# Performance work log

Measured on AMD Instinct MI355X. Metric: run time of the kernel, lower is better.

Reference implementation:

```python
import jax, jax.numpy as jnp
import numpy as np

N_WORDS = 500000
N_LABELS = 64
PAD_INDEX = 0
UNK_INDEX = 1
BATCH, SEQ_LEN = 8192, 512


def setup_inputs() -> dict:
    key = jax.random.key(0)
    kw, kl, klen = jax.random.split(key, 3)
    # sequence lengths in [S/2, S]; pads go at the end (loop semantics assume contiguous prefix)
    lens = jax.random.randint(klen, (BATCH,), SEQ_LEN // 2, SEQ_LEN + 1)
    words = jax.random.randint(kw, (BATCH, SEQ_LEN), 2, N_WORDS, dtype=jnp.int32)
    labels = jax.random.randint(kl, (BATCH, SEQ_LEN), 0, N_LABELS, dtype=jnp.int32)
    pos = jnp.arange(SEQ_LEN, dtype=jnp.int32)[None, :]
    words = jnp.where(pos < lens[:, None], words, PAD_INDEX)
    trans_count = jnp.zeros((N_LABELS + 1, N_LABELS + 1), jnp.float32)
    emit_count = jnp.zeros((N_WORDS, N_LABELS), jnp.float32)
    return {"words": words, "labels": labels,
            "trans_count": trans_count, "emit_count": emit_count}


def reference(words, labels, trans_count, emit_count):
    # Vectorized equivalent of the double Python loop of scalar increments.
    B, S = words.shape
    lens = (words != PAD_INDEX).sum(-1)                       # [B]
    valid = jnp.arange(S, dtype=lens.dtype)[None, :] < lens[:, None]  # [B,S]
    wgt = valid.astype(trans_count.dtype).ravel()             # 1.0 for counted tokens
    ext_words = jnp.where(words >= N_WORDS, UNK_INDEX, words)
    # pre label: -1 (== last index N_LABELS) at j=0, else labels[:, j-1]
    pre = jnp.concatenate(
        [jnp.full((B, 1), N_LABELS, labels.dtype), labels[:, :-1]], axis=1)
    # trans_count[t, pre] += 1  (flattened scatter-add)
    t_flat = (labels.astype(jnp.int32) * (N_LABELS + 1) + pre.astype(jnp.int32)).ravel()
    tc = trans_count.ravel().at[t_flat].add(wgt).reshape(trans_count.shape)
    # emit_count[w, t] += 1
    e_flat = (ext_words.astype(jnp.int32) * N_LABELS + labels.astype(jnp.int32)).ravel()
    ec = emit_count.ravel().at[e_flat].add(wgt).reshape(emit_count.shape)
    return tc, ec
```

## Files before the change

### kernel.cpp

```cpp
#include <hip/hip_runtime.h>
#include <hip/hip_bf16.h>


constexpr int N_WORDS  = 500000;
constexpr int N_LABELS = 64;
constexpr int SEQ_LEN  = 512;
constexpr int BINS     = (N_LABELS + 1) * (N_LABELS + 1);
constexpr int N_CELLS  = N_WORDS * N_LABELS;
constexpr int P        = 1025;
constexpr int CPP      = 31232;
constexpr int CAP      = 8192;
constexpr int B1 = 1024, G1 = 512;
constexpr int TILE_TOK = 8192;
constexpr int B2 = 1024;
constexpr int FIN_BLOCKS = 5;


__global__ __launch_bounds__(B1)
void phase1(const int* __restrict__ words, const int* __restrict__ labels,
            unsigned* __restrict__ cursors,
            unsigned short* __restrict__ keys,
            unsigned* __restrict__ part_t,
            int n) {
    __shared__ unsigned trans[BINS];
    __shared__ unsigned keybuf[TILE_TOK];
    __shared__ unsigned cnt[P];
    __shared__ unsigned base[P];
    __shared__ unsigned pos[P];
    for (int k = threadIdx.x; k < BINS; k += B1) trans[k] = 0u;
    __syncthreads();

    const int nquads = n >> 2;
    const int qpt    = TILE_TOK >> 2;
    const int ntiles = (nquads + qpt - 1) / qpt;

    for (int tile = blockIdx.x; tile < ntiles; tile += gridDim.x) {
        const int q0     = tile * qpt;
        const int tquads = min(qpt, nquads - q0);

        for (int k = threadIdx.x; k < P; k += B1) { cnt[k] = 0u; pos[k] = 0u; }
        __syncthreads();

        for (int lq = threadIdx.x; lq < tquads; lq += B1) {
            const int q = q0 + lq;
            const int i = q << 2;
            const int4 w4 = reinterpret_cast<const int4*>(words)[q];
            const int4 l4 = reinterpret_cast<const int4*>(labels)[q];
            const int j0 = i & (SEQ_LEN - 1);
            int pre = (j0 == 0) ? N_LABELS : labels[i - 1];
            int wv[4] = {w4.x, w4.y, w4.z, w4.w};
            int lv[4] = {l4.x, l4.y, l4.z, l4.w};
            #pragma unroll
            for (int k = 0; k < 4; ++k) {
                const int lab = lv[k];
                unsigned pack = 0xFFFFFFFFu;
                if (wv[k] != 0) {
                    atomicAdd(&trans[lab * (N_LABELS + 1) + pre], 1u);
                    const int w = (wv[k] >= N_WORDS) ? 1 : wv[k];
                    const unsigned key = (unsigned)w * N_LABELS + (unsigned)lab;
                    const unsigned p   = key / CPP;
                    pack = (p << 16) | (key - p * CPP);
                    atomicAdd(&cnt[p], 1u);
                }
                keybuf[(lq << 2) + k] = pack;
                pre = lab;
            }
        }
        __syncthreads();

        for (int p = threadIdx.x; p < P; p += B1) {
            const unsigned c = cnt[p];
            base[p] = c ? atomicAdd(&cursors[p], c) : 0u;
        }
        __syncthreads();

        const int ttok = tquads << 2;
        for (int t = threadIdx.x; t < ttok; t += B1) {
            const unsigned pack = keybuf[t];
            if (pack != 0xFFFFFFFFu) {
                const unsigned p   = pack >> 16;
                const unsigned loc = pack & 0xFFFFu;
                const unsigned slot = base[p] + atomicAdd(&pos[p], 1u);
                if (slot < CAP)
                    keys[(size_t)p * CAP + slot] = (unsigned short)loc;
            }
        }
        __syncthreads();
    }

    unsigned* my = part_t + (size_t)blockIdx.x * BINS;
    for (int k = threadIdx.x; k < BINS; k += B1) my[k] = trans[k];
}


__global__ __launch_bounds__(B2)
void phase2(const unsigned* __restrict__ cursors,
            const unsigned short* __restrict__ keys,
            const unsigned* __restrict__ part_t,
            float* __restrict__ out) {
    extern __shared__ unsigned h[];
    const unsigned bid = blockIdx.x;

    if (bid >= (unsigned)P) {
        const int k = (bid - P) * B2 + threadIdx.x;
        if (k < BINS) {
            unsigned s = 0;
            #pragma unroll 8
            for (int pb = 0; pb < G1; ++pb) s += part_t[(size_t)pb * BINS + k];
            out[k] = (float)s;
        }
        return;
    }

    float* __restrict__ emit = out + BINS;
    const unsigned base_cell = bid * (unsigned)CPP;
    const unsigned cells = min((unsigned)CPP, (unsigned)N_CELLS - base_cell);
    const unsigned n32 = (cells + 1u) >> 1;
    unsigned nk = cursors[bid]; if (nk > CAP) nk = CAP;
    const unsigned short* kp = keys + (size_t)bid * CAP;

    for (unsigned j = threadIdx.x; j < n32; j += B2) h[j] = 0u;
    __syncthreads();
    for (unsigned i = threadIdx.x; i < nk; i += B2) {
        const unsigned c = kp[i];
        atomicAdd(&h[c >> 1], (c & 1u) ? 65536u : 1u);
    }
    __syncthreads();
    for (unsigned j = threadIdx.x; j < cells; j += B2) {
        const unsigned v = h[j >> 1];
        const unsigned c = (j & 1u) ? (v >> 16) : (v & 0xFFFFu);
        emit[base_cell + j] = (float)c;
    }
}


__global__ __launch_bounds__(256)
void zero_kernel(uint4* __restrict__ out, int out_quads, int out_size) {
    const uint4 z = {0u, 0u, 0u, 0u};
    const int stride = gridDim.x * blockDim.x;
    for (int q = blockIdx.x * blockDim.x + threadIdx.x; q < out_quads; q += stride)
        out[q] = z;
    if (blockIdx.x == 0 && threadIdx.x < (out_size & 3))
        ((unsigned*)out)[(out_quads << 2) + threadIdx.x] = 0u;
}

__global__ __launch_bounds__(1024)
void count_fallback(const int* __restrict__ words, const int* __restrict__ labels,
                    float* __restrict__ out, int nquads) {
    __shared__ unsigned hist[BINS];
    for (int k = threadIdx.x; k < BINS; k += 1024) hist[k] = 0u;
    __syncthreads();
    float* __restrict__ emit = out + BINS;
    const int stride = gridDim.x * blockDim.x;
    for (int q = blockIdx.x * blockDim.x + threadIdx.x; q < nquads; q += stride) {
        const int i = q << 2;
        const int4 w4 = reinterpret_cast<const int4*>(words)[q];
        const int4 l4 = reinterpret_cast<const int4*>(labels)[q];
        const int j0 = i & (SEQ_LEN - 1);
        int pre = (j0 == 0) ? N_LABELS : labels[i - 1];
        int wv[4] = {w4.x, w4.y, w4.z, w4.w};
        int lv[4] = {l4.x, l4.y, l4.z, l4.w};
        #pragma unroll
        for (int k = 0; k < 4; ++k) {
            const int w = wv[k], lab = lv[k];
            if (w != 0) {
                atomicAdd(&hist[lab * (N_LABELS + 1) + pre], 1u);
                const int we = (w >= N_WORDS) ? 1 : w;
                atomicAdd(&emit[(size_t)we * N_LABELS + lab], 1.0f);
            }
            pre = lab;
        }
    }
    __syncthreads();
    for (int k = threadIdx.x; k < 1024 * 8 && k < BINS; k += 1024) {}
    for (int k = threadIdx.x; k < BINS; k += 1024) {
        const unsigned c = hist[k];
        if (c) atomicAdd(&out[k], (float)c);
    }
}


extern "C" void kernel_launch(void* const* d_in, const int* in_sizes, int n_in,
                              void* d_out, int out_size, void* d_ws, size_t ws_size,
                              hipStream_t stream) {
    const int* words  = (const int*)d_in[0];
    const int* labels = (const int*)d_in[1];
    float* out = (float*)d_out;

    const int n = in_sizes[0];

    const size_t cur_off   = 0;
    const size_t key_off   = 8192;
    const size_t key_bytes = (size_t)P * CAP * sizeof(unsigned short);
    const size_t part_off  = key_off + key_bytes;
    const size_t part_bytes = (size_t)G1 * BINS * sizeof(unsigned);
    const size_t need = part_off + part_bytes;

    if (ws_size >= need) {
        unsigned* cursors    = (unsigned*)((char*)d_ws + cur_off);
        unsigned short* keys = (unsigned short*)((char*)d_ws + key_off);
        unsigned* part_t     = (unsigned*)((char*)d_ws + part_off);

        hipMemsetAsync(cursors, 0, P * sizeof(unsigned), stream);
        phase1<<<G1, B1, 0, stream>>>(words, labels, cursors, keys, part_t, n);
        phase2<<<P + FIN_BLOCKS, B2, (CPP / 2) * sizeof(unsigned), stream>>>(
            cursors, keys, part_t, out);
    } else {
        const int out_quads = out_size >> 2;
        zero_kernel<<<2048, 256, 0, stream>>>((uint4*)d_out, out_quads, out_size);
        count_fallback<<<512, 1024, 0, stream>>>(words, labels, out, n >> 2);
    }
}
```

Before: 273.9 us.

## Fuse bucketing and histogram phases into one cooperative kernel with grid sync

Replaces the memset plus two kernel launches with a single cooperative kernel. It zeroes the cursors, buckets the keys, does a grid-wide sync, and then builds per-partition LDS histograms with float4 output stores. The partition count changes to 1000 with 32000 cells each, and the grid is sized from occupancy. This removes launch overhead and the tail between phases, at the cost of fewer resident blocks during the histogram phase and the expense of grid syncs. The large dynamic LDS is now also allocated during phase 1.

```diff
diff --git a/kernel.cpp b/kernel.cpp
--- a/kernel.cpp
+++ b/kernel.cpp
@@ -1,47 +1,54 @@
 #include <hip/hip_runtime.h>
-#include <hip/hip_bf16.h>
+#include <hip/hip_cooperative_groups.h>
+
+namespace cg = cooperative_groups;
 
 
 constexpr int N_WORDS  = 500000;
 constexpr int N_LABELS = 64;
 constexpr int SEQ_LEN  = 512;
 constexpr int BINS     = (N_LABELS + 1) * (N_LABELS + 1);
-constexpr int N_CELLS  = N_WORDS * N_LABELS;
-constexpr int P        = 1025;
-constexpr int CPP      = 31232;
+constexpr int P        = 1000;
+constexpr int CPP      = 32000;
 constexpr int CAP      = 8192;
-constexpr int B1 = 1024, G1 = 512;
+constexpr int B        = 1024;
+constexpr int MAXG     = 512;
 constexpr int TILE_TOK = 8192;
-constexpr int B2 = 1024;
-constexpr int FIN_BLOCKS = 5;
-
-
-__global__ __launch_bounds__(B1)
-void phase1(const int* __restrict__ words, const int* __restrict__ labels,
-            unsigned* __restrict__ cursors,
-            unsigned short* __restrict__ keys,
-            unsigned* __restrict__ part_t,
-            int n) {
-    __shared__ unsigned trans[BINS];
-    __shared__ unsigned keybuf[TILE_TOK];
-    __shared__ unsigned cnt[P];
-    __shared__ unsigned base[P];
-    __shared__ unsigned pos[P];
-    for (int k = threadIdx.x; k < BINS; k += B1) trans[k] = 0u;
-    __syncthreads();
+constexpr int QPT      = TILE_TOK / 4;
+constexpr size_t DYN_BYTES = (size_t)(CPP / 2) * 4;
+
+
+__global__ __launch_bounds__(B)
+void fused(const int* __restrict__ words, const int* __restrict__ labels,
+           unsigned* __restrict__ cursors,
+           unsigned short* __restrict__ keys,
+           unsigned* __restrict__ part_t,
+           float* __restrict__ out, int n) {
+    extern __shared__ unsigned dyn[];
+    cg::grid_group grid = cg::this_grid();
+    const int tid = threadIdx.x, bid = blockIdx.x, G = gridDim.x;
+
+    for (int c = bid * B + tid; c < P; c += G * B) cursors[c] = 0u;
+    grid.sync();
+
+    unsigned* keybuf = dyn;
+    unsigned* trans  = dyn + 8192;
+    unsigned* cnt    = dyn + 8192 + BINS;
+    unsigned* base_  = cnt + 1024;
+    unsigned* pos    = base_ + 1024;
+
+    for (int k = tid; k < BINS; k += B) trans[k] = 0u;
 
     const int nquads = n >> 2;
-    const int qpt    = TILE_TOK >> 2;
-    const int ntiles = (nquads + qpt - 1) / qpt;
-
-    for (int tile = blockIdx.x; tile < ntiles; tile += gridDim.x) {
-        const int q0     = tile * qpt;
-        const int tquads = min(qpt, nquads - q0);
-
-        for (int k = threadIdx.x; k < P; k += B1) { cnt[k] = 0u; pos[k] = 0u; }
-        __syncthreads();
-
-        for (int lq = threadIdx.x; lq < tquads; lq += B1) {
+    const int ntiles = (nquads + QPT - 1) / QPT;
+
+    for (int tile = bid; tile < ntiles; tile += G) {
+        const int q0 = tile * QPT;
+        const int tq = min(QPT, nquads - q0);
+        for (int k = tid; k < P; k += B) { cnt[k] = 0u; pos[k] = 0u; }
+        __syncthreads();
+
+        for (int lq = tid; lq < tq; lq += B) {
             const int q = q0 + lq;
             const int i = q << 2;
             const int4 w4 = reinterpret_cast<const int4*>(words)[q];
@@ -50,6 +57,7 @@
             int pre = (j0 == 0) ? N_LABELS : labels[i - 1];
             int wv[4] = {w4.x, w4.y, w4.z, w4.w};
             int lv[4] = {l4.x, l4.y, l4.z, l4.w};
+            unsigned pk[4];
             #pragma unroll
             for (int k = 0; k < 4; ++k) {
                 const int lab = lv[k];
@@ -62,25 +70,27 @@
                     pack = (p << 16) | (key - p * CPP);
                     atomicAdd(&cnt[p], 1u);
                 }
-                keybuf[(lq << 2) + k] = pack;
+                pk[k] = pack;
                 pre = lab;
             }
-        }
-        __syncthreads();
-
-        for (int p = threadIdx.x; p < P; p += B1) {
+            reinterpret_cast<uint4*>(keybuf)[lq] =
+                make_uint4(pk[0], pk[1], pk[2], pk[3]);
+        }
+        __syncthreads();
+
+        for (int p = tid; p < P; p += B) {
             const unsigned c = cnt[p];
-            base[p] = c ? atomicAdd(&cursors[p], c) : 0u;
-        }
-        __syncthreads();
-
-        const int ttok = tquads << 2;
-        for (int t = threadIdx.x; t < ttok; t += B1) {
+            base_[p] = c ? atomicAdd(&cursors[p], c) : 0u;
+        }
+        __syncthreads();
+
+        const int tt = tq << 2;
+        for (int t = tid; t < tt; t += B) {
             const unsigned pack = keybuf[t];
             if (pack != 0xFFFFFFFFu) {
-                const unsigned p   = pack >> 16;
-                const unsigned loc = pack & 0xFFFFu;
-                const unsigned slot = base[p] + atomicAdd(&pos[p], 1u);
+                const unsigned p    = pack >> 16;
+                const unsigned loc  = pack & 0xFFFFu;
+                const unsigned slot = base_[p] + atomicAdd(&pos[p], 1u);
                 if (slot < CAP)
                     keys[(size_t)p * CAP + slot] = (unsigned short)loc;
             }
@@ -88,48 +98,45 @@
         __syncthreads();
     }
 
-    unsigned* my = part_t + (size_t)blockIdx.x * BINS;
-    for (int k = threadIdx.x; k < BINS; k += B1) my[k] = trans[k];
-}
-
-
-__global__ __launch_bounds__(B2)
-void phase2(const unsigned* __restrict__ cursors,
-            const unsigned short* __restrict__ keys,
-            const unsigned* __restrict__ part_t,
-            float* __restrict__ out) {
-    extern __shared__ unsigned h[];
-    const unsigned bid = blockIdx.x;
-
-    if (bid >= (unsigned)P) {
-        const int k = (bid - P) * B2 + threadIdx.x;
-        if (k < BINS) {
-            unsigned s = 0;
-            #pragma unroll 8
-            for (int pb = 0; pb < G1; ++pb) s += part_t[(size_t)pb * BINS + k];
-            out[k] = (float)s;
-        }
-        return;
-    }
+    {
+        unsigned* my = part_t + (size_t)bid * BINS;
+        for (int k = tid; k < BINS; k += B) my[k] = trans[k];
+    }
+    grid.sync();
 
     float* __restrict__ emit = out + BINS;
-    const unsigned base_cell = bid * (unsigned)CPP;
-    const unsigned cells = min((unsigned)CPP, (unsigned)N_CELLS - base_cell);
-    const unsigned n32 = (cells + 1u) >> 1;
-    unsigned nk = cursors[bid]; if (nk > CAP) nk = CAP;
-    const unsigned short* kp = keys + (size_t)bid * CAP;
-
-    for (unsigned j = threadIdx.x; j < n32; j += B2) h[j] = 0u;
-    __syncthreads();
-    for (unsigned i = threadIdx.x; i < nk; i += B2) {
-        const unsigned c = kp[i];
-        atomicAdd(&h[c >> 1], (c & 1u) ? 65536u : 1u);
-    }
-    __syncthreads();
-    for (unsigned j = threadIdx.x; j < cells; j += B2) {
-        const unsigned v = h[j >> 1];
-        const unsigned c = (j & 1u) ? (v >> 16) : (v & 0xFFFFu);
-        emit[base_cell + j] = (float)c;
+    for (int p = bid; p < P; p += G) {
+        for (int j = tid; j < CPP / 2; j += B) dyn[j] = 0u;
+        __syncthreads();
+        unsigned nk = cursors[p]; if (nk > CAP) nk = CAP;
+        const unsigned short* kp = keys + (size_t)p * CAP;
+        for (unsigned i = tid; i < nk; i += B)
+            atomicAdd(&dyn[kp[i] >> 1], (kp[i] & 1u) ? 65536u : 1u);
+        __syncthreads();
+        float* dst = emit + (size_t)p * CPP;
+        if (tid < 3)
+            dst[tid] = (float)((dyn[tid >> 1] >> ((tid & 1u) * 16)) & 0xFFFFu);
+        if (tid == 3)
+            dst[CPP - 1] = (float)(dyn[(CPP - 1) >> 1] >> 16);
+        float4* dst4 = reinterpret_cast<float4*>(dst + 3);
+        for (int u = tid; u < (CPP - 4) / 4; u += B) {
+            const unsigned w0 = dyn[2 * u + 1];
+            const unsigned w1 = dyn[2 * u + 2];
+            const unsigned w2 = dyn[2 * u + 3];
+            float4 f;
+            f.x = (float)(w0 >> 16);
+            f.y = (float)(w1 & 0xFFFFu);
+            f.z = (float)(w1 >> 16);
+            f.w = (float)(w2 & 0xFFFFu);
+            dst4[u] = f;
+        }
+        __syncthreads();
+    }
+
+    for (int k = bid * B + tid; k < BINS; k += G * B) {
+        unsigned s = 0;
+        for (int pb = 0; pb < G; ++pb) s += part_t[(size_t)pb * BINS + k];
+        out[k] = (float)s;
     }
 }
 
@@ -172,7 +179,6 @@
         }
     }
     __syncthreads();
-    for (int k = threadIdx.x; k < 1024 * 8 && k < BINS; k += 1024) {}
     for (int k = threadIdx.x; k < BINS; k += 1024) {
         const unsigned c = hist[k];
         if (c) atomicAdd(&out[k], (float)c);
@@ -186,26 +192,39 @@
     const int* words  = (const int*)d_in[0];
     const int* labels = (const int*)d_in[1];
     float* out = (float*)d_out;
-
     const int n = in_sizes[0];
 
-    const size_t cur_off   = 0;
-    const size_t key_off   = 8192;
-    const size_t key_bytes = (size_t)P * CAP * sizeof(unsigned short);
-    const size_t part_off  = key_off + key_bytes;
-    const size_t part_bytes = (size_t)G1 * BINS * sizeof(unsigned);
-    const size_t need = part_off + part_bytes;
-
+    const size_t key_off    = 4096;
+    const size_t key_bytes  = (size_t)P * CAP * sizeof(unsigned short);
+    const size_t part_off   = key_off + key_bytes;
+    const size_t part_bytes = (size_t)MAXG * BINS * sizeof(unsigned);
+    const size_t need       = part_off + part_bytes;
+
+    static int G = 0;
+    if (G == 0) {
+        int nb = 0;
+        if (hipOccupancyMaxActiveBlocksPerMultiprocessor(
+                &nb, (const void*)fused, B, DYN_BYTES) != hipSuccess || nb < 1)
+            nb = 1;
+        int dev = 0; hipGetDevice(&dev);
+        hipDeviceProp_t prop;
+        int cus = (hipGetDeviceProperties(&prop, dev) == hipSuccess)
+                      ? prop.multiProcessorCount : 256;
+        int g = nb * cus;
+        G = g < 1 ? 1 : (g > MAXG ? MAXG : g);
+    }
+
+    bool ok = false;
     if (ws_size >= need) {
-        unsigned* cursors    = (unsigned*)((char*)d_ws + cur_off);
+        unsigned* cursors    = (unsigned*)d_ws;
         unsigned short* keys = (unsigned short*)((char*)d_ws + key_off);
         unsigned* part_t     = (unsigned*)((char*)d_ws + part_off);
-
-        hipMemsetAsync(cursors, 0, P * sizeof(unsigned), stream);
-        phase1<<<G1, B1, 0, stream>>>(words, labels, cursors, keys, part_t, n);
-        phase2<<<P + FIN_BLOCKS, B2, (CPP / 2) * sizeof(unsigned), stream>>>(
-            cursors, keys, part_t, out);
-    } else {
+        void* args[] = {(void*)&words, (void*)&labels, (void*)&cursors,
+                        (void*)&keys, (void*)&part_t, (void*)&out, (void*)&n};
+        ok = (hipLaunchCooperativeKernel((const void*)fused, dim3(G), dim3(B),
+                                         args, DYN_BYTES, stream) == hipSuccess);
+    }
+    if (!ok) {
         const int out_quads = out_size >> 2;
         zero_kernel<<<2048, 256, 0, stream>>>((uint4*)d_out, out_quads, out_size);
         count_fallback<<<512, 1024, 0, stream>>>(words, labels, out, n >> 2);
```

New measurement: 352.9 us. 1.29x slower.

## Replace global partition cursors with per-tile sorted key segments and directory

Applied to the files above, without the earlier changes.

Phase1 no longer does global atomics on partition cursors. Each 4096-token tile now counting-sorts its keys in shared memory with a block-wide scan, writes them contiguously, and records a per-tile (count, offset) directory. A transpose kernel reorders the directory by partition. Phase2 then walks each partition's segments across all tiles and writes the output with float4 stores. This removes global atomic contention and scattered 2-byte writes, and drops the CAP overflow limit, at the cost of an extra kernel, a serial scan, and irregular per-thread segment loops in phase2.

```diff
diff --git a/kernel.cpp b/kernel.cpp
--- a/kernel.cpp
+++ b/kernel.cpp
@@ -7,42 +7,39 @@
 constexpr int SEQ_LEN  = 512;
 constexpr int BINS     = (N_LABELS + 1) * (N_LABELS + 1);
 constexpr int N_CELLS  = N_WORDS * N_LABELS;
-constexpr int P        = 1025;
-constexpr int CPP      = 31232;
-constexpr int CAP      = 8192;
+constexpr int P        = 1000;
+constexpr int CPP      = 32000;
+constexpr int TILE_TOK = 4096;
+constexpr int QPT      = TILE_TOK / 4;
 constexpr int B1 = 1024, G1 = 512;
-constexpr int TILE_TOK = 8192;
 constexpr int B2 = 1024;
 constexpr int FIN_BLOCKS = 5;
 
 
 __global__ __launch_bounds__(B1)
 void phase1(const int* __restrict__ words, const int* __restrict__ labels,
-            unsigned* __restrict__ cursors,
+            unsigned* __restrict__ dir,
             unsigned short* __restrict__ keys,
             unsigned* __restrict__ part_t,
-            int n) {
+            int n, int ntiles) {
     __shared__ unsigned trans[BINS];
     __shared__ unsigned keybuf[TILE_TOK];
-    __shared__ unsigned cnt[P];
-    __shared__ unsigned base[P];
-    __shared__ unsigned pos[P];
-    for (int k = threadIdx.x; k < BINS; k += B1) trans[k] = 0u;
-    __syncthreads();
+    __shared__ unsigned short sorted[TILE_TOK];
+    __shared__ unsigned cnt[1024];
+    __shared__ unsigned scanbuf[1024];
+    __shared__ unsigned cursor[1024];
+    const int tid = threadIdx.x;
+    for (int k = tid; k < BINS; k += B1) trans[k] = 0u;
 
     const int nquads = n >> 2;
-    const int qpt    = TILE_TOK >> 2;
-    const int ntiles = (nquads + qpt - 1) / qpt;
-
     for (int tile = blockIdx.x; tile < ntiles; tile += gridDim.x) {
-        const int q0     = tile * qpt;
-        const int tquads = min(qpt, nquads - q0);
-
-        for (int k = threadIdx.x; k < P; k += B1) { cnt[k] = 0u; pos[k] = 0u; }
-        __syncthreads();
-
-        for (int lq = threadIdx.x; lq < tquads; lq += B1) {
-            const int q = q0 + lq;
+        const int q0 = tile * QPT;
+        const int tq = min(QPT, nquads - q0);
+        cnt[tid] = 0u;
+        __syncthreads();
+
+        if (tid < tq) {
+            const int q = q0 + tid;
             const int i = q << 2;
             const int4 w4 = reinterpret_cast<const int4*>(words)[q];
             const int4 l4 = reinterpret_cast<const int4*>(labels)[q];
@@ -50,6 +47,7 @@
             int pre = (j0 == 0) ? N_LABELS : labels[i - 1];
             int wv[4] = {w4.x, w4.y, w4.z, w4.w};
             int lv[4] = {l4.x, l4.y, l4.z, l4.w};
+            unsigned pk[4];
             #pragma unroll
             for (int k = 0; k < 4; ++k) {
                 const int lab = lv[k];
@@ -62,42 +60,70 @@
                     pack = (p << 16) | (key - p * CPP);
                     atomicAdd(&cnt[p], 1u);
                 }
-                keybuf[(lq << 2) + k] = pack;
+                pk[k] = pack;
                 pre = lab;
             }
-        }
-        __syncthreads();
-
-        for (int p = threadIdx.x; p < P; p += B1) {
-            const unsigned c = cnt[p];
-            base[p] = c ? atomicAdd(&cursors[p], c) : 0u;
-        }
-        __syncthreads();
-
-        const int ttok = tquads << 2;
-        for (int t = threadIdx.x; t < ttok; t += B1) {
+            reinterpret_cast<uint4*>(keybuf)[tid] = make_uint4(pk[0], pk[1], pk[2], pk[3]);
+        }
+        __syncthreads();
+
+        const unsigned myc = cnt[tid];
+        unsigned v = myc;
+        #pragma unroll
+        for (int d = 1; d < 1024; d <<= 1) {
+            scanbuf[tid] = v; __syncthreads();
+            if (tid >= d) v += scanbuf[tid - d];
+            __syncthreads();
+        }
+        const unsigned off = v - myc;
+        cursor[tid] = off;
+        if (tid < P) dir[(size_t)tile * P + tid] = (myc << 16) | off;
+        __syncthreads();
+
+        const int tt = tq << 2;
+        for (int t = tid; t < tt; t += B1) {
             const unsigned pack = keybuf[t];
             if (pack != 0xFFFFFFFFu) {
-                const unsigned p   = pack >> 16;
-                const unsigned loc = pack & 0xFFFFu;
-                const unsigned slot = base[p] + atomicAdd(&pos[p], 1u);
-                if (slot < CAP)
-                    keys[(size_t)p * CAP + slot] = (unsigned short)loc;
+                const unsigned s = atomicAdd(&cursor[pack >> 16], 1u);
+                sorted[s] = (unsigned short)(pack & 0xFFFFu);
             }
         }
         __syncthreads();
+
+        if (tid < TILE_TOK / 8)
+            reinterpret_cast<uint4*>(keys + (size_t)tile * TILE_TOK)[tid] =
+                reinterpret_cast<const uint4*>(sorted)[tid];
+        __syncthreads();
     }
 
     unsigned* my = part_t + (size_t)blockIdx.x * BINS;
-    for (int k = threadIdx.x; k < BINS; k += B1) my[k] = trans[k];
+    for (int k = tid; k < BINS; k += B1) my[k] = trans[k];
+}
+
+
+__global__ __launch_bounds__(256)
+void transpose_dir(const unsigned* __restrict__ dir, unsigned* __restrict__ dirT,
+                   int ntiles, int tstride) {
+    __shared__ unsigned tb[32][33];
+    const int p0 = blockIdx.x * 32, t0 = blockIdx.y * 32;
+    const int tx = threadIdx.x, ty = threadIdx.y;
+    for (int j = ty; j < 32; j += 8) {
+        const int t = t0 + j, p = p0 + tx;
+        tb[j][tx] = (t < ntiles && p < P) ? dir[(size_t)t * P + p] : 0u;
+    }
+    __syncthreads();
+    for (int j = ty; j < 32; j += 8) {
+        const int p = p0 + j, t = t0 + tx;
+        if (p < P && t < tstride) dirT[(size_t)p * tstride + t] = tb[tx][j];
+    }
 }
 
 
 __global__ __launch_bounds__(B2)
-void phase2(const unsigned* __restrict__ cursors,
+void phase2(const unsigned* __restrict__ dirT,
             const unsigned short* __restrict__ keys,
             const unsigned* __restrict__ part_t,
-            float* __restrict__ out) {
+            float* __restrict__ out, int ntiles, int tstride) {
     extern __shared__ unsigned h[];
     const unsigned bid = blockIdx.x;
 
@@ -112,24 +138,39 @@
         return;
     }
 
+    for (int j = threadIdx.x; j < CPP / 2; j += B2) h[j] = 0u;
+    __syncthreads();
+
+    const unsigned* drow = dirT + (size_t)bid * tstride;
+    for (int t = threadIdx.x; t < ntiles; t += B2) {
+        const unsigned e = drow[t];
+        unsigned c = e >> 16;
+        const unsigned short* kp = keys + (size_t)t * TILE_TOK + (e & 0xFFFFu);
+        for (unsigned i = 0; i < c; ++i) {
+            const unsigned loc = kp[i];
+            atomicAdd(&h[loc >> 1], (loc & 1u) ? 65536u : 1u);
+        }
+    }
+    __syncthreads();
+
     float* __restrict__ emit = out + BINS;
-    const unsigned base_cell = bid * (unsigned)CPP;
-    const unsigned cells = min((unsigned)CPP, (unsigned)N_CELLS - base_cell);
-    const unsigned n32 = (cells + 1u) >> 1;
-    unsigned nk = cursors[bid]; if (nk > CAP) nk = CAP;
-    const unsigned short* kp = keys + (size_t)bid * CAP;
-
-    for (unsigned j = threadIdx.x; j < n32; j += B2) h[j] = 0u;
-    __syncthreads();
-    for (unsigned i = threadIdx.x; i < nk; i += B2) {
-        const unsigned c = kp[i];
-        atomicAdd(&h[c >> 1], (c & 1u) ? 65536u : 1u);
-    }
-    __syncthreads();
-    for (unsigned j = threadIdx.x; j < cells; j += B2) {
-        const unsigned v = h[j >> 1];
-        const unsigned c = (j & 1u) ? (v >> 16) : (v & 0xFFFFu);
-        emit[base_cell + j] = (float)c;
+    float* dst = emit + (size_t)bid * CPP;
+    if (threadIdx.x < 3)
+        dst[threadIdx.x] =
+            (float)((h[threadIdx.x >> 1] >> ((threadIdx.x & 1u) * 16)) & 0xFFFFu);
+    if (threadIdx.x == 3)
+        dst[CPP - 1] = (float)(h[(CPP - 1) >> 1] >> 16);
+    float4* dst4 = reinterpret_cast<float4*>(dst + 3);
+    for (int u = threadIdx.x; u < (CPP - 4) / 4; u += B2) {
+        const unsigned w0 = h[2 * u + 1];
+        const unsigned w1 = h[2 * u + 2];
+        const unsigned w2 = h[2 * u + 3];
+        float4 f;
+        f.x = (float)(w0 >> 16);
+        f.y = (float)(w1 & 0xFFFFu);
+        f.z = (float)(w1 >> 16);
+        f.w = (float)(w2 & 0xFFFFu);
+        dst4[u] = f;
     }
 }
 
@@ -172,7 +213,6 @@
         }
     }
     __syncthreads();
-    for (int k = threadIdx.x; k < 1024 * 8 && k < BINS; k += 1024) {}
     for (int k = threadIdx.x; k < BINS; k += 1024) {
         const unsigned c = hist[k];
         if (c) atomicAdd(&out[k], (float)c);
@@ -186,28 +226,36 @@
     const int* words  = (const int*)d_in[0];
     const int* labels = (const int*)d_in[1];
     float* out = (float*)d_out;
-
     const int n = in_sizes[0];
 
-    const size_t cur_off   = 0;
-    const size_t key_off   = 8192;
-    const size_t key_bytes = (size_t)P * CAP * sizeof(unsigned short);
-    const size_t part_off  = key_off + key_bytes;
+    const int nquads  = n >> 2;
+    const int ntiles  = (nquads + QPT - 1) / QPT;
+    const int tstride = ((ntiles + 63) / 64) * 64;
+
+    const size_t dir_bytes  = (size_t)ntiles * P * sizeof(unsigned);
+    const size_t dirT_bytes = (size_t)P * tstride * sizeof(unsigned);
+    const size_t key_bytes  = (size_t)ntiles * TILE_TOK * sizeof(unsigned short);
     const size_t part_bytes = (size_t)G1 * BINS * sizeof(unsigned);
-    const size_t need = part_off + part_bytes;
+    const size_t dir_off  = 0;
+    const size_t dirT_off = dir_off + ((dir_bytes + 255) & ~size_t(255));
+    const size_t key_off  = dirT_off + ((dirT_bytes + 255) & ~size_t(255));
+    const size_t part_off = key_off + ((key_bytes + 255) & ~size_t(255));
+    const size_t need     = part_off + part_bytes;
 
     if (ws_size >= need) {
-        unsigned* cursors    = (unsigned*)((char*)d_ws + cur_off);
-        unsigned short* keys = (unsigned short*)((char*)d_ws + key_off);
-        unsigned* part_t     = (unsigned*)((char*)d_ws + part_off);
-
-        hipMemsetAsync(cursors, 0, P * sizeof(unsigned), stream);
-        phase1<<<G1, B1, 0, stream>>>(words, labels, cursors, keys, part_t, n);
+        unsigned*       dir    = (unsigned*)((char*)d_ws + dir_off);
+        unsigned*       dirT   = (unsigned*)((char*)d_ws + dirT_off);
+        unsigned short* keys   = (unsigned short*)((char*)d_ws + key_off);
+        unsigned*       part_t = (unsigned*)((char*)d_ws + part_off);
+
+        phase1<<<G1, B1, 0, stream>>>(words, labels, dir, keys, part_t, n, ntiles);
+        dim3 tg((P + 31) / 32, (tstride + 31) / 32);
+        transpose_dir<<<tg, dim3(32, 8), 0, stream>>>(dir, dirT, ntiles, tstride);
         phase2<<<P + FIN_BLOCKS, B2, (CPP / 2) * sizeof(unsigned), stream>>>(
-            cursors, keys, part_t, out);
+            dirT, keys, part_t, out, ntiles, tstride);
     } else {
         const int out_quads = out_size >> 2;
         zero_kernel<<<2048, 256, 0, stream>>>((uint4*)d_out, out_quads, out_size);
-        count_fallback<<<512, 1024, 0, stream>>>(words, labels, out, n >> 2);
-    }
-}
+        count_fallback<<<512, 1024, 0, stream>>>(words, labels, out, nquads);
+    }
+}
```

After: 266.5 us. -2.7%, faster.
